# Performance work log

Measured on AMD Instinct MI355X. Metric: run time of the kernel, lower is better.

## Reference

```python
import jax, jax.numpy as jnp
from jax import lax
import numpy as np

H = 32  # hidden_size

def setup_inputs() -> dict:
    key = jax.random.key(0)
    ks = jax.random.split(key, 7)
    B, T = 32, 16384
    s = 1.0 / np.sqrt(H)  # torch LSTM/Linear init scale
    x = jax.random.normal(ks[0], (B, T, 1), dtype=jnp.float32)
    W_ih = jax.random.uniform(ks[1], (4 * H, 1), jnp.float32, -s, s)
    W_hh = jax.random.uniform(ks[2], (4 * H, H), jnp.float32, -s, s)
    b_ih = jax.random.uniform(ks[3], (4 * H,), jnp.float32, -s, s)
    b_hh = jax.random.uniform(ks[4], (4 * H,), jnp.float32, -s, s)
    W_out = jax.random.uniform(ks[5], (1, H), jnp.float32, -s, s)
    b_out = jax.random.uniform(ks[6], (1,), jnp.float32, -s, s)
    return {"x": x, "W_ih": W_ih, "W_hh": W_hh, "b_ih": b_ih,
            "b_hh": b_hh, "W_out": W_out, "b_out": b_out}

def reference(x, W_ih, W_hh, b_ih, b_hh, W_out, b_out):
    B, T, _ = x.shape
    # Precompute input contribution to all gates once: (B, T, 4H)
    pre = jnp.einsum('bti,gi->btg', x, W_ih) + b_ih + b_hh

    def step(carry, p_t):
        h, c = carry
        gates = p_t + h @ W_hh.T  # (B, 4H), torch gate order i,f,g,o
        i, f, g, o = jnp.split(gates, 4, axis=-1)
        c = jax.nn.sigmoid(f) * c + jax.nn.sigmoid(i) * jnp.tanh(g)
        h = jax.nn.sigmoid(o) * jnp.tanh(c)
        return (h, c), h

    h0 = jnp.zeros((B, H), x.dtype)
    (_, _), hs = lax.scan(step, (h0, h0), jnp.swapaxes(pre, 0, 1))
    hs = jnp.swapaxes(hs, 0, 1)  # (B, T, H)
    return hs @ W_out.T + b_out  # (B, T, 1)
```

## Files before the change

kernel.cpp:

```cpp
#include <hip/hip_runtime.h>

#define T_LEN 16384
#define BATCH 32
#define HID 32
#define L2E 1.44269504088896340736f
#define SCLG (-2.0f * 1.44269504088896340736f)

typedef float f2 __attribute__((ext_vector_type(2)));
typedef unsigned u2_t __attribute__((ext_vector_type(2)));

#if __has_builtin(__builtin_amdgcn_exp2f)
#define EXP2F(x) __builtin_amdgcn_exp2f(x)
#else
#define EXP2F(x) __exp2f(x)
#endif
#if __has_builtin(__builtin_amdgcn_rcpf)
#define RCPF(x) __builtin_amdgcn_rcpf(x)
#else
#define RCPF(x) (1.0f / (x))
#endif

__device__ __forceinline__ float rlane(float v, int lane) {
    return __int_as_float(__builtin_amdgcn_readlane(__float_as_int(v), lane));
}

__device__ __forceinline__ float xhalf_lo_to_hi(float v) {
#if __has_builtin(__builtin_amdgcn_permlane32_swap)
    u2_t r = __builtin_amdgcn_permlane32_swap(__float_as_uint(v), __float_as_uint(v),
                                              false, false);
    return __uint_as_float(r.x);
#else
    return __shfl_xor(v, 32, 64);
#endif
}

__global__ __launch_bounds__(64) __attribute__((amdgpu_waves_per_eu(1, 1)))
void lstm_seq_kernel(const float* __restrict__ x,
                     const float* __restrict__ W_ih,
                     const float* __restrict__ W_hh,
                     const float* __restrict__ b_ih,
                     const float* __restrict__ b_hh,
                     const float* __restrict__ W_out,
                     const float* __restrict__ b_out,
                     float* __restrict__ out)
{
    const int b    = blockIdx.x;
    const int lane = threadIdx.x;
    const int j    = lane & 31;
    const bool upper = (lane >= 32);

    const int rowA = upper ? (32 + j) : j;
    const int rowB = upper ? (96 + j) : (64 + j);

    const float sclA = -L2E;
    const float sclB = upper ? -L2E : SCLG;

    f2 Wa2[16], Wb2[16];
    const f2* ra2 = reinterpret_cast<const f2*>(W_hh + (size_t)rowA * HID);
    const f2* rb2 = reinterpret_cast<const f2*>(W_hh + (size_t)rowB * HID);
    #pragma unroll
    for (int q = 0; q < 16; ++q) { Wa2[q] = ra2[q] * sclA; Wb2[q] = rb2[q] * sclB; }
    #pragma unroll
    for (int q = 0; q < 16; ++q) { asm("" : "+v"(Wa2[q]), "+v"(Wb2[q])); }

    const float wihA = sclA * W_ih[rowA];
    const float wihB = sclB * W_ih[rowB];
    const float bA = sclA * (b_ih[rowA] + b_hh[rowA]);
    const float bB = sclB * (b_ih[rowB] + b_hh[rowB]);

    const float wout = W_out[j];
    const float bout = b_out[0];

    __shared__ float phist[64 * 65];

    float cS = 0.0f;

    f2 hp[16];
    #pragma unroll
    for (int p = 0; p < 16; ++p) hp[p] = (f2){0.0f, 0.0f};

    const float* xb = x + (size_t)b * T_LEN;
    float*       yb = out + (size_t)b * T_LEN;

    float xv = xb[lane];

    for (int t0 = 0; t0 < T_LEN; t0 += 64) {
        float xv_next = (t0 + 64 < T_LEN) ? xb[t0 + 64 + lane] : 0.0f;

        #pragma unroll 4
        for (int s = 0; s < 64; ++s) {
            const float xs  = rlane(xv, s);
            const float xpA = fmaf(xs, wihA, bA);
            const float xpB = fmaf(xs, wihB, bB);

            f2 zA[4], zB[4];
            zA[0].x = xpA; zA[0].y = 0.0f;
            zB[0].x = xpB; zB[0].y = 0.0f;
            #pragma unroll
            for (int p = 0; p < 16; ++p) {
                if (p == 0) {
                    asm("v_pk_fma_f32 %0, %1, %2, %0"
                        : "+v"(zA[0]) : "s"(hp[0]), "v"(Wa2[0]));
                    asm("v_pk_fma_f32 %0, %1, %2, %0"
                        : "+v"(zB[0]) : "s"(hp[0]), "v"(Wb2[0]));
                } else if (p < 4) {
                    asm("v_pk_mul_f32 %0, %1, %2"
                        : "=v"(zA[p]) : "s"(hp[p]), "v"(Wa2[p]));
                    asm("v_pk_mul_f32 %0, %1, %2"
                        : "=v"(zB[p]) : "s"(hp[p]), "v"(Wb2[p]));
                } else {
                    asm("v_pk_fma_f32 %0, %1, %2, %0"
                        : "+v"(zA[p & 3]) : "s"(hp[p]), "v"(Wa2[p]));
                    asm("v_pk_fma_f32 %0, %1, %2, %0"
                        : "+v"(zB[p & 3]) : "s"(hp[p]), "v"(Wb2[p]));
                }
            }
            const f2 rA = (zA[0] + zA[1]) + (zA[2] + zA[3]);
            const f2 rB = (zB[0] + zB[1]) + (zB[2] + zB[3]);
            const float za = rA.x + rA.y;
            const float zb = rB.x + rB.y;

            const float A = RCPF(1.0f + EXP2F(za));
            const float r = RCPF(1.0f + EXP2F(zb));
            const float tgS = fmaf(r, 2.0f * SCLG, -SCLG);
            const float so2 = r + r;

            const float up = A * tgS;
            const float tu = xhalf_lo_to_hi(up);

            cS = fmaf(A, cS, tu);
            const float r2 = RCPF(1.0f + EXP2F(cS));
            const float h  = fmaf(so2, r2, -r);

            #pragma unroll
            for (int p = 0; p < 16; ++p) {
                f2 t;
                t.x = rlane(h, 32 + 2 * p);
                t.y = rlane(h, 33 + 2 * p);
                hp[p] = t;
            }

            phist[s * 65 + lane] = h * wout;
        }

        __syncthreads();
        float a0 = bout, a1 = 0.0f, a2 = 0.0f, a3 = 0.0f;
        #pragma unroll
        for (int k = 0; k < HID; k += 4) {
            a0 += phist[lane * 65 + 32 + k];
            a1 += phist[lane * 65 + 33 + k];
            a2 += phist[lane * 65 + 34 + k];
            a3 += phist[lane * 65 + 35 + k];
        }
        yb[t0 + lane] = (a0 + a1) + (a2 + a3);
        __syncthreads();

        xv = xv_next;
    }
}

extern "C" void kernel_launch(void* const* d_in, const int* in_sizes, int n_in,
                              void* d_out, int out_size, void* d_ws, size_t ws_size,
                              hipStream_t stream) {
    const float* x     = (const float*)d_in[0];
    const float* W_ih  = (const float*)d_in[1];
    const float* W_hh  = (const float*)d_in[2];
    const float* b_ih  = (const float*)d_in[3];
    const float* b_hh  = (const float*)d_in[4];
    const float* W_out = (const float*)d_in[5];
    const float* b_out = (const float*)d_in[6];
    float* out = (float*)d_out;

    lstm_seq_kernel<<<BATCH, 64, 0, stream>>>(x, W_ih, W_hh, b_ih, b_hh,
                                              W_out, b_out, out);
}
```

Measured before the change: 3.545 ms.

## Broadcast hidden state via DPP/permlane butterfly instead of 32 readlanes

Replaces the per-step broadcast of the hidden state (32 v_readlane into SGPRs) with a butterfly all-gather built from permlane16/permlane32 swaps and DPP moves. Each lane then holds all 32 h values in VGPRs, in a lane-specific order, and W_hh columns are permuted at load time to match. The cell update is also made symmetric across both half-waves so that both halves compute c and h. The aim is to avoid the serialized readlane/SGPR dependency chain on the recurrence critical path. In exchange it adds about 31 DPP ops per step and some extra VGPR pressure, and it relies on selx correctly detecting the permlane16 swap semantics.

After: 3.793 ms. 1.07x slower.

```diff
diff --git a/kernel.cpp b/kernel.cpp
--- a/kernel.cpp
+++ b/kernel.cpp
@@ -24,14 +24,50 @@
     return __int_as_float(__builtin_amdgcn_readlane(__float_as_int(v), lane));
 }
 
-__device__ __forceinline__ float xhalf_lo_to_hi(float v) {
+__device__ __forceinline__ u2_t xswap32(unsigned a, unsigned b) {
 #if __has_builtin(__builtin_amdgcn_permlane32_swap)
-    u2_t r = __builtin_amdgcn_permlane32_swap(__float_as_uint(v), __float_as_uint(v),
-                                              false, false);
-    return __uint_as_float(r.x);
-#else
-    return __shfl_xor(v, 32, 64);
-#endif
+    return __builtin_amdgcn_permlane32_swap(a, b, false, false);
+#else
+    u2_t r;
+    r.x = __shfl_xor(b, 32, 64);
+    r.y = __shfl_xor(a, 32, 64);
+    return r;
+#endif
+}
+
+#define DPP(v, ctrl) ((unsigned)__builtin_amdgcn_mov_dpp((int)(v), (ctrl), 0xF, 0xF, true))
+
+struct H32 {
+    f2 p[16];
+    __device__ __forceinline__ unsigned get(int i) const {
+        return __float_as_uint((i & 1) ? p[i >> 1].y : p[i >> 1].x);
+    }
+    __device__ __forceinline__ void set(int i, unsigned u) {
+        if (i & 1) p[i >> 1].y = __uint_as_float(u);
+        else       p[i >> 1].x = __uint_as_float(u);
+    }
+};
+
+__device__ __forceinline__ void gather32(H32& o, unsigned h0, bool selx) {
+    unsigned p16;
+#if __has_builtin(__builtin_amdgcn_permlane16_swap)
+    {
+        u2_t rr = __builtin_amdgcn_permlane16_swap(h0, h0, false, false);
+        p16 = selx ? rr.x : rr.y;
+    }
+#else
+    p16 = (unsigned)__builtin_amdgcn_ds_swizzle((int)h0, 0x401F);
+#endif
+    o.set(0, h0);
+    o.set(1, p16);
+    #pragma unroll
+    for (int k = 0; k < 2; ++k)  o.set(2 + k,  DPP(o.get(k), 0xB1));
+    #pragma unroll
+    for (int k = 0; k < 4; ++k)  o.set(4 + k,  DPP(o.get(k), 0x4E));
+    #pragma unroll
+    for (int k = 0; k < 8; ++k)  o.set(8 + k,  DPP(o.get(k), 0x124));
+    #pragma unroll
+    for (int k = 0; k < 16; ++k) o.set(16 + k, DPP(o.get(k), 0x128));
 }
 
 __global__ __launch_bounds__(64) __attribute__((amdgpu_waves_per_eu(1, 1)))
@@ -55,11 +91,28 @@
     const float sclA = -L2E;
     const float sclB = upper ? -L2E : SCLG;
 
+    bool selx = false;
+#if __has_builtin(__builtin_amdgcn_permlane16_swap)
+    {
+        u2_t rr = __builtin_amdgcn_permlane16_swap((unsigned)lane, (unsigned)lane,
+                                                   false, false);
+        selx = (rr.x == (unsigned)(lane ^ 16));
+    }
+#endif
+
+    H32 cols;
+    gather32(cols, (unsigned)j, selx);
+
     f2 Wa2[16], Wb2[16];
-    const f2* ra2 = reinterpret_cast<const f2*>(W_hh + (size_t)rowA * HID);
-    const f2* rb2 = reinterpret_cast<const f2*>(W_hh + (size_t)rowB * HID);
-    #pragma unroll
-    for (int q = 0; q < 16; ++q) { Wa2[q] = ra2[q] * sclA; Wb2[q] = rb2[q] * sclB; }
+    #pragma unroll
+    for (int q = 0; q < 16; ++q) {
+        const int c0 = (int)cols.get(2 * q);
+        const int c1 = (int)cols.get(2 * q + 1);
+        Wa2[q].x = W_hh[rowA * HID + c0] * sclA;
+        Wa2[q].y = W_hh[rowA * HID + c1] * sclA;
+        Wb2[q].x = W_hh[rowB * HID + c0] * sclB;
+        Wb2[q].y = W_hh[rowB * HID + c1] * sclB;
+    }
     #pragma unroll
     for (int q = 0; q < 16; ++q) { asm("" : "+v"(Wa2[q]), "+v"(Wb2[q])); }
 
@@ -75,9 +128,9 @@
 
     float cS = 0.0f;
 
-    f2 hp[16];
-    #pragma unroll
-    for (int p = 0; p < 16; ++p) hp[p] = (f2){0.0f, 0.0f};
+    H32 hs;
+    #pragma unroll
+    for (int q = 0; q < 16; ++q) hs.p[q] = (f2){0.0f, 0.0f};
 
     const float* xb = x + (size_t)b * T_LEN;
     float*       yb = out + (size_t)b * T_LEN;
@@ -100,19 +153,19 @@
             for (int p = 0; p < 16; ++p) {
                 if (p == 0) {
                     asm("v_pk_fma_f32 %0, %1, %2, %0"
-                        : "+v"(zA[0]) : "s"(hp[0]), "v"(Wa2[0]));
-                    asm("v_pk_fma_f32 %0, %1, %2, %0"
-                        : "+v"(zB[0]) : "s"(hp[0]), "v"(Wb2[0]));
+                        : "+v"(zA[0]) : "v"(hs.p[0]), "v"(Wa2[0]));
+                    asm("v_pk_fma_f32 %0, %1, %2, %0"
+                        : "+v"(zB[0]) : "v"(hs.p[0]), "v"(Wb2[0]));
                 } else if (p < 4) {
                     asm("v_pk_mul_f32 %0, %1, %2"
-                        : "=v"(zA[p]) : "s"(hp[p]), "v"(Wa2[p]));
+                        : "=v"(zA[p]) : "v"(hs.p[p]), "v"(Wa2[p]));
                     asm("v_pk_mul_f32 %0, %1, %2"
-                        : "=v"(zB[p]) : "s"(hp[p]), "v"(Wb2[p]));
+                        : "=v"(zB[p]) : "v"(hs.p[p]), "v"(Wb2[p]));
                 } else {
                     asm("v_pk_fma_f32 %0, %1, %2, %0"
-                        : "+v"(zA[p & 3]) : "s"(hp[p]), "v"(Wa2[p]));
-                    asm("v_pk_fma_f32 %0, %1, %2, %0"
-                        : "+v"(zB[p & 3]) : "s"(hp[p]), "v"(Wb2[p]));
+                        : "+v"(zA[p & 3]) : "v"(hs.p[p]), "v"(Wa2[p]));
+                    asm("v_pk_fma_f32 %0, %1, %2, %0"
+                        : "+v"(zB[p & 3]) : "v"(hs.p[p]), "v"(Wb2[p]));
                 }
             }
             const f2 rA = (zA[0] + zA[1]) + (zA[2] + zA[3]);
@@ -126,19 +179,18 @@
             const float so2 = r + r;
 
             const float up = A * tgS;
-            const float tu = xhalf_lo_to_hi(up);
-
-            cS = fmaf(A, cS, tu);
+
+            const u2_t s1 = xswap32(__float_as_uint(A), __float_as_uint(up));
+            const u2_t s2 = xswap32(__float_as_uint(so2), __float_as_uint(so2));
+            const float F    = upper ? A : __uint_as_float(s1.y);
+            const float U    = upper ? __uint_as_float(s1.x) : up;
+            const float so2a = __uint_as_float(s2.y);
+
+            cS = fmaf(F, cS, U);
             const float r2 = RCPF(1.0f + EXP2F(cS));
-            const float h  = fmaf(so2, r2, -r);
-
-            #pragma unroll
-            for (int p = 0; p < 16; ++p) {
-                f2 t;
-                t.x = rlane(h, 32 + 2 * p);
-                t.y = rlane(h, 33 + 2 * p);
-                hp[p] = t;
-            }
+            const float h  = so2a * (r2 - 0.5f);
+
+            gather32(hs, __float_as_uint(h), selx);
 
             phist[s * 65 + lane] = h * wout;
         }
```
